# Kernel optimization log

Measured on AMD Instinct MI355X. Metric: run time of the kernel, lower is better.

Reference implementation:

```python
import jax, jax.numpy as jnp
import numpy as np

NUM_HEADS = 16
DIM = 1024


def setup_inputs() -> dict:
    key = jax.random.key(0)
    k1, k2, k3, k4 = jax.random.split(key, 4)
    B, N, C = 4, 2048, DIM
    x = jax.random.normal(k1, (B, N, C), dtype=jnp.float32)
    # weights stored in apply orientation: y = x @ W (+ b)
    W_qkv = jax.random.normal(k2, (C, 3 * C), dtype=jnp.float32) * (C ** -0.5)
    W_out = jax.random.normal(k3, (C, C), dtype=jnp.float32) * (C ** -0.5)
    b_out = jax.random.normal(k4, (C,), dtype=jnp.float32) * 0.01
    return {"hidden_states": x, "W_qkv": W_qkv, "W_out": W_out, "b_out": b_out}


def reference(hidden_states, W_qkv, W_out, b_out):
    B, N, C = hidden_states.shape
    H = NUM_HEADS
    Dh = C // H
    scale = Dh ** -0.5
    qkv = hidden_states @ W_qkv                      # [B, N, 3C]
    qkv = qkv.reshape(B, N, 3, H, Dh).transpose(2, 0, 3, 1, 4)  # [3, B, H, N, Dh]
    q, k, v = qkv[0], qkv[1], qkv[2]
    scores = jnp.einsum('bhnd,bhmd->bhnm', q, k) * scale  # [B, H, N, N]
    probs = jax.nn.softmax(scores, axis=-1)
    out = jnp.einsum('bhnm,bhmd->bhnd', probs, v)    # [B, H, N, Dh]
    out = out.transpose(0, 2, 1, 3).reshape(B, N, C)  # merge heads
    return out @ W_out + b_out                        # dropout p=0 -> identity
```

## Files before the change

kernel.cpp:

```cpp
#include <hip/hip_runtime.h>
#include <hip/hip_bf16.h>
#include <stdint.h>

#define BATCH 4
#define SEQN  2048
#define DIMC  1024
#define NHEADS 16
#define DHEAD 64
#define BH_TOT 64
#define MROWS 8192

typedef __attribute__((ext_vector_type(8))) short bf16x8;
typedef __attribute__((ext_vector_type(4))) float f32x4;

__device__ __forceinline__ unsigned short bf16_rtne(float f){
  union { float f; unsigned u; } v; v.f = f;
  unsigned u = v.u;
  return (unsigned short)((u + 0x7FFFu + ((u >> 16) & 1u)) >> 16);
}
__device__ __forceinline__ float bf16f(unsigned short h){
  union { unsigned u; float f; } v; v.u = ((unsigned)h) << 16;
  return v.f;
}
__device__ __forceinline__ unsigned cvt_pk_bf16(float lo, float hi){
  unsigned r;
  asm("v_cvt_pk_bf16_f32 %0, %1, %2" : "=v"(r) : "v"(lo), "v"(hi));
  return r;
}

__device__ __forceinline__ void async16(void* lds, const void* g){
  __builtin_amdgcn_global_load_lds((const __attribute__((address_space(1))) void*)g,
                                   (__attribute__((address_space(3))) void*)lds, 16, 0, 0);
}

__global__ __launch_bounds__(256) void split_rows_k(const float* __restrict__ X,
    unsigned short* __restrict__ O, int nrows, int Kc){
  int q4 = Kc >> 2;
  int total = nrows * q4;
  int idx = blockIdx.x*256 + threadIdx.x;
  if (idx >= total) return;
  int row = idx / q4, c = idx - row*q4;
  const float4 v = *(const float4*)(X + ((size_t)row*Kc + c*4));
  float fv[4] = {v.x, v.y, v.z, v.w};
  unsigned short hi[4], lo[4];
#pragma unroll
  for (int j=0;j<4;j++){ hi[j] = bf16_rtne(fv[j]); lo[j] = bf16_rtne(fv[j] - bf16f(hi[j])); }
  size_t ob = (size_t)row*(2*Kc) + c*4;
  ushort4 h; h.x=hi[0]; h.y=hi[1]; h.z=hi[2]; h.w=hi[3];
  ushort4 l2; l2.x=lo[0]; l2.y=lo[1]; l2.z=lo[2]; l2.w=lo[3];
  *(ushort4*)(O + ob) = h;
  *(ushort4*)(O + ob + Kc) = l2;
}

__global__ __launch_bounds__(256) void transpose_split_k(const float* __restrict__ W,
    unsigned short* __restrict__ Wt, int K, int Nc){
  __shared__ float tile[32][33];
  int tx = threadIdx.x & 31, ty = threadIdx.x >> 5;
  int n0 = blockIdx.x*32, k0 = blockIdx.y*32;
#pragma unroll
  for (int i=0;i<4;i++){
    int k = k0 + ty + i*8;
    tile[ty + i*8][tx] = W[(size_t)k*Nc + n0 + tx];
  }
  __syncthreads();
#pragma unroll
  for (int i=0;i<4;i++){
    int n = n0 + ty + i*8;
    float f = tile[tx][ty + i*8];
    unsigned short hi = bf16_rtne(f);
    unsigned short lo = bf16_rtne(f - bf16f(hi));
    Wt[(size_t)n*(2*K) + k0 + tx] = hi;
    Wt[(size_t)n*(2*K) + K + k0 + tx] = lo;
  }
}

__global__ __launch_bounds__(512, 4) void gemm_split_k(
    const unsigned short* __restrict__ A, const unsigned short* __restrict__ Bt,
    float* __restrict__ C, const float* __restrict__ bias, int M, int Nc, int K)
{
  __shared__ unsigned short a_lds[3*8192];
  __shared__ unsigned short b_lds[3*4096];
  const int t = threadIdx.x, wid = t>>6, l = t&63, lg = l>>4, ll = l&15;
  const int wm = wid>>1, wn = wid&1;
  const int nbm = M>>8;
  const int nwg = nbm*(Nc>>7);
  const int orig = blockIdx.x;
  const int id = ((orig&7)*(nwg>>3)) + (orig>>3);
  const int m0 = (id % nbm)<<8, n0 = (id / nbm)<<7;
  const int ldk = 2*K;
  const int nkt = (3*K)>>5;
  f32x4 acc[4][4];
#pragma unroll
  for (int i=0;i<4;i++)
#pragma unroll
    for (int j=0;j<4;j++) acc[i][j] = (f32x4){0.f,0.f,0.f,0.f};

  auto stageA = [&](int wb, int kt2){
    const int kp = kt2<<5;
    const int ac = (kp < K) ? kp : kp - K;
#pragma unroll
    for (int i=0;i<2;i++){
      int b = i*8 + wid;
      async16(&a_lds[wb*8192 + b*512 + l*8],
              A + (size_t)(m0 + b*16 + ll)*ldk + ac + lg*8);
    }
  };
  auto stageB = [&](int wb, int kt2){
    const int kp = kt2<<5;
    const int bc = (kp < 2*K) ? kp : kp - 2*K;
    async16(&b_lds[wb*4096 + wid*512 + l*8],
            Bt + (size_t)(n0 + wid*16 + ll)*ldk + bc + lg*8);
  };

  stageA(0, 0); stageB(0, 0);
  stageA(1, 1); stageB(1, 1);

  for (int kt=0; kt<nkt; ++kt){
    if (kt < nkt-1) asm volatile("s_waitcnt vmcnt(3)\n\ts_barrier" ::: "memory");
    else            asm volatile("s_waitcnt vmcnt(0)\n\ts_barrier" ::: "memory");
    const int rb = kt % 3;
    const unsigned short* ab = &a_lds[rb*8192];
    const unsigned short* bb = &b_lds[rb*4096];
    bf16x8 af[4], bf[4];
#pragma unroll
    for (int i=0;i<4;i++) af[i] = *(const bf16x8*)&ab[(wm*4+i)*512 + l*8];
#pragma unroll
    for (int j=0;j<4;j++) bf[j] = *(const bf16x8*)&bb[(wn*4+j)*512 + l*8];
    if (kt+2 < nkt){
      const int wb = (kt+2) % 3;
      stageA(wb, kt+2); stageB(wb, kt+2);
    }
    __builtin_amdgcn_s_setprio(1);
#pragma unroll
    for (int i=0;i<4;i++)
#pragma unroll
      for (int j=0;j<4;j++)
        acc[i][j] = __builtin_amdgcn_mfma_f32_16x16x32_bf16(af[i], bf[j], acc[i][j], 0,0,0);
    __builtin_amdgcn_s_setprio(0);
  }

#pragma unroll
  for (int i=0;i<4;i++)
#pragma unroll
    for (int j=0;j<4;j++){
      int col = n0 + wn*64 + j*16 + ll;
      float bv = bias ? bias[col] : 0.f;
#pragma unroll
      for (int r=0;r<4;r++){
        int row = m0 + wm*64 + i*16 + lg*4 + r;
        C[(size_t)row*Nc + col] = acc[i][j][r] + bv;
      }
    }
}

#define QSCALE 0.18033688f
__global__ __launch_bounds__(256) void split_qk_k(const float* __restrict__ qkv,
    unsigned short* __restrict__ Qo, unsigned short* __restrict__ Ko){
  int idx = blockIdx.x*256 + threadIdx.x;
  int d4 = idx & 15, n = (idx>>4) & (SEQN-1), bh = idx >> 15;
  int b = bh>>4, h = bh&15;
  size_t base = ((size_t)(b*SEQN + n))*3072 + h*64 + d4*4;
  float4 q = *(const float4*)(qkv + base);
  float4 k = *(const float4*)(qkv + base + 1024);
  float fq[4] = {q.x*QSCALE, q.y*QSCALE, q.z*QSCALE, q.w*QSCALE};
  float fk[4] = {k.x, k.y, k.z, k.w};
  unsigned short qh[4], ql[4], kh[4];
#pragma unroll
  for (int j=0;j<4;j++){
    qh[j] = bf16_rtne(fq[j]); ql[j] = bf16_rtne(fq[j] - bf16f(qh[j]));
    kh[j] = bf16_rtne(fk[j]);
  }
  size_t obq = ((size_t)bh*SEQN + n)*128 + d4*4;
  size_t obk = ((size_t)bh*SEQN + n)*64 + d4*4;
  ushort4 u;
  u.x=qh[0];u.y=qh[1];u.z=qh[2];u.w=qh[3]; *(ushort4*)(Qo+obq) = u;
  u.x=ql[0];u.y=ql[1];u.z=ql[2];u.w=ql[3]; *(ushort4*)(Qo+obq+64) = u;
  u.x=kh[0];u.y=kh[1];u.z=kh[2];u.w=kh[3]; *(ushort4*)(Ko+obk) = u;
}

__global__ __launch_bounds__(256) void build_vt_k(const float* __restrict__ qkv,
    unsigned short* __restrict__ Vt){
  __shared__ float tile[64][65];
  const int mt = blockIdx.x, bh = blockIdx.y;
  const int b = bh>>4, h = bh&15;
  const int t = threadIdx.x;
  const int r = t>>2, seg = t&3;
  size_t src = ((size_t)(b*SEQN + mt*64 + r))*3072 + 2048 + h*64 + seg*16;
#pragma unroll
  for (int j=0;j<4;j++){
    float4 v = *(const float4*)(qkv + src + j*4);
    tile[r][seg*16 + j*4 + 0] = v.x;
    tile[r][seg*16 + j*4 + 1] = v.y;
    tile[r][seg*16 + j*4 + 2] = v.z;
    tile[r][seg*16 + j*4 + 3] = v.w;
  }
  __syncthreads();
  const int d = r, ms = seg;
  unsigned short o16[16];
#pragma unroll
  for (int j=0;j<16;j++) o16[j] = bf16_rtne(tile[ms*16 + j][d]);
  size_t dst = ((size_t)(bh*64 + d))*SEQN + mt*64 + ms*16;
  uint4 u0, u1;
  unsigned* pu = (unsigned*)&u0;
  unsigned* pv = (unsigned*)&u1;
#pragma unroll
  for (int j=0;j<4;j++){
    pu[j] = (unsigned)o16[2*j]   | ((unsigned)o16[2*j+1]<<16);
    pv[j] = (unsigned)o16[8+2*j] | ((unsigned)o16[9+2*j]<<16);
  }
  *(uint4*)(Vt + dst) = u0;
  *(uint4*)(Vt + dst + 8) = u1;
}

__global__ __launch_bounds__(256, 4) void attn_k(const unsigned short* __restrict__ Q,
    const unsigned short* __restrict__ Kh, const unsigned short* __restrict__ Vt,
    unsigned short* __restrict__ att_hl)
{
  __shared__ unsigned short k_lds[2][4096];
  __shared__ unsigned short v_lds[2][4096];
  __shared__ unsigned p_lds[4][512];
  const int orig = blockIdx.y*gridDim.x + blockIdx.x;
  const int id = ((orig & 7) << 8) + (orig >> 3);
  const int qt = id & 31, bh = id >> 5;
  const int b = bh>>4, h = bh&15;
  const int t = threadIdx.x, w = t>>6, l = t&63, lg = l>>4, ll = l&15;
  const size_t kvbase = (size_t)bh*SEQN;

  bf16x8 qf[4];
  {
    size_t qrow = (kvbase + qt*64 + w*16 + ll) * 128;
#pragma unroll
    for (int i=0;i<4;i++)
      qf[i] = *(const bf16x8*)(Q + qrow + i*32 + lg*8);
  }
  f32x4 o[4];
#pragma unroll
  for (int d=0; d<4; d++) o[d] = (f32x4){0.f,0.f,0.f,0.f};
  float lsum = 0.f;

  auto stage = [&](int buf, int kv){
    int m0 = kv*64;
#pragma unroll
    for (int i=0;i<2;i++){
      int s = t + i*256; int row = s>>3; int sl = s&7; int sl2 = sl ^ (row&7);
      async16(&k_lds[buf][s*8], Kh + (kvbase + m0 + row)*64 + sl2*8);
    }
#pragma unroll
    for (int i=0;i<2;i++){
      int s = t + i*256; int row = s>>3; int sl = s&7; int sl2 = sl ^ (row&7);
      async16(&v_lds[buf][s*8], Vt + ((size_t)bh*64 + row)*SEQN + m0 + sl2*8);
    }
  };

  stage(0, 0);
  __syncthreads();
  const int NKV = SEQN/64;
  for (int kv=0; kv<NKV; ++kv){
    int cur = kv&1;
    if (kv+1 < NKV) stage(cur^1, kv+1);
#pragma unroll
    for (int nt=0; nt<4; ++nt){
      int row = nt*16 + ll;
      bf16x8 kf0 = *(const bf16x8*)&k_lds[cur][row*64 + (((0*4+lg) ^ (row&7))*8)];
      bf16x8 kf1 = *(const bf16x8*)&k_lds[cur][row*64 + (((1*4+lg) ^ (row&7))*8)];
      f32x4 a = (f32x4){0.f,0.f,0.f,0.f};
      __builtin_amdgcn_s_setprio(1);
      a = __builtin_amdgcn_mfma_f32_16x16x32_bf16(kf0, qf[0], a, 0,0,0);
      a = __builtin_amdgcn_mfma_f32_16x16x32_bf16(kf1, qf[1], a, 0,0,0);
      a = __builtin_amdgcn_mfma_f32_16x16x32_bf16(kf0, qf[2], a, 0,0,0);
      a = __builtin_amdgcn_mfma_f32_16x16x32_bf16(kf1, qf[3], a, 0,0,0);
      __builtin_amdgcn_s_setprio(0);
      float e0 = exp2f(a[0]), e1 = exp2f(a[1]), e2 = exp2f(a[2]), e3 = exp2f(a[3]);
      lsum += (e0 + e1) + (e2 + e3);
      unsigned pk0 = cvt_pk_bf16(e0, e1);
      unsigned pk1 = cvt_pk_bf16(e2, e3);
      int c0 = nt*8 + lg*2;
      int addr = ll*32 + (((c0>>2) ^ (ll&7))<<2) + (c0&3);
      *(uint2*)&p_lds[w][addr] = make_uint2(pk0, pk1);
    }
#pragma unroll
    for (int ks=0; ks<2; ++ks){
      int chunk = ks*4 + lg;
      bf16x8 pf = *(const bf16x8*)&p_lds[w][ll*32 + ((chunk ^ (ll&7))<<2)];
      __builtin_amdgcn_s_setprio(1);
#pragma unroll
      for (int dt=0; dt<4; ++dt){
        int row = dt*16 + ll;
        bf16x8 vf = *(const bf16x8*)&v_lds[cur][row*64 + (((ks*4+lg) ^ (row&7))*8)];
        o[dt] = __builtin_amdgcn_mfma_f32_16x16x32_bf16(pf, vf, o[dt], 0,0,0);
      }
      __builtin_amdgcn_s_setprio(0);
    }
    __syncthreads();
  }
  float tot = lsum;
  tot += __shfl_xor(tot, 16);
  tot += __shfl_xor(tot, 32);
  float inv = 1.0f / tot;
#pragma unroll
  for (int r=0;r<4;r++){
    float rl = __shfl(inv, lg*4 + r);
    int qrow = qt*64 + w*16 + lg*4 + r;
    size_t ob = ((size_t)(b*SEQN + qrow))*2048 + h*64;
#pragma unroll
    for (int dt=0; dt<4; ++dt){
      float f = o[dt][r] * rl;
      unsigned short hi = bf16_rtne(f);
      unsigned short lo = bf16_rtne(f - bf16f(hi));
      att_hl[ob + dt*16 + ll] = hi;
      att_hl[ob + 1024 + dt*16 + ll] = lo;
    }
  }
}

extern "C" void kernel_launch(void* const* d_in, const int* in_sizes, int n_in,
                              void* d_out, int out_size, void* d_ws, size_t ws_size,
                              hipStream_t stream){
  const float* x    = (const float*)d_in[0];
  const float* Wqkv = (const float*)d_in[1];
  const float* Wout = (const float*)d_in[2];
  const float* bout = (const float*)d_in[3];
  float* out = (float*)d_out;

  char* ws = (char*)d_ws;
  size_t off = 0;
  auto walloc = [&](size_t bytes) -> void* {
    void* p = ws + off; off += (bytes + 255) & ~(size_t)255; return p;
  };
  unsigned short* x_hl   = (unsigned short*)walloc((size_t)MROWS*2048*2);
  unsigned short* wqkv_t = (unsigned short*)walloc((size_t)3072*2048*2);
  float*          qkv    = (float*)walloc((size_t)MROWS*3072*4);
  unsigned short* q_hl   = (unsigned short*)walloc((size_t)BH_TOT*SEQN*128*2);
  unsigned short* k_h    = (unsigned short*)walloc((size_t)BH_TOT*SEQN*64*2);
  unsigned short* vt     = (unsigned short*)walloc((size_t)BH_TOT*64*SEQN*2);
  unsigned short* wout_t = (unsigned short*)walloc((size_t)1024*2048*2);
  unsigned short* att_hl = x_hl;

  split_rows_k<<<8192, 256, 0, stream>>>(x, x_hl, MROWS, DIMC);
  transpose_split_k<<<dim3(3072/32, 1024/32), 256, 0, stream>>>(Wqkv, wqkv_t, 1024, 3072);
  transpose_split_k<<<dim3(1024/32, 1024/32), 256, 0, stream>>>(Wout, wout_t, 1024, 1024);
  gemm_split_k<<<768, 512, 0, stream>>>(x_hl, wqkv_t, qkv, nullptr, MROWS, 3072, 1024);
  split_qk_k<<<(BH_TOT*SEQN*16)/256, 256, 0, stream>>>(qkv, q_hl, k_h);
  build_vt_k<<<dim3(SEQN/64, BH_TOT), 256, 0, stream>>>(qkv, vt);
  attn_k<<<dim3(SEQN/64, BH_TOT), 256, 0, stream>>>(q_hl, k_h, vt, att_hl);
  gemm_split_k<<<256, 512, 0, stream>>>(att_hl, wout_t, out, bout, MROWS, 1024, 1024);
}
```

Measured before the change: 559.5 us.

## Retile split-bf16 GEMM to 128x256 tiles with K=64 double-buffered staging

Changes the split-precision GEMM from 256x128 tiles with a 3-stage K=32 ring to 128x256 tiles with K=64 steps and double buffering. A and B loads are interleaved across two half-steps separated by an extra barrier. The warp layout becomes 2x4, and occupancy is lowered to 2 workgroups per CU to fit the larger LDS footprint. The goal is fewer loop iterations and barriers per unit of MFMA work, at the cost of a shallower pipeline and lower occupancy.

New measurement: 556.8 us. Within noise of the previous version (-0.5%).

```diff
diff --git a/kernel.cpp b/kernel.cpp
--- a/kernel.cpp
+++ b/kernel.cpp
@@ -74,81 +74,116 @@
   }
 }
 
-__global__ __launch_bounds__(512, 4) void gemm_split_k(
+__global__ __launch_bounds__(512, 2) void gemm_split_k(
     const unsigned short* __restrict__ A, const unsigned short* __restrict__ Bt,
     float* __restrict__ C, const float* __restrict__ bias, int M, int Nc, int K)
 {
-  __shared__ unsigned short a_lds[3*8192];
-  __shared__ unsigned short b_lds[3*4096];
+  __shared__ unsigned short a_lds[2][8192];
+  __shared__ unsigned short b_lds[2][16384];
   const int t = threadIdx.x, wid = t>>6, l = t&63, lg = l>>4, ll = l&15;
-  const int wm = wid>>1, wn = wid&1;
-  const int nbm = M>>8;
-  const int nwg = nbm*(Nc>>7);
+  const int wm = wid>>2, wn = wid&3;
+  const int nbm = M>>7;
+  const int nwg = nbm*(Nc>>8);
   const int orig = blockIdx.x;
   const int id = ((orig&7)*(nwg>>3)) + (orig>>3);
-  const int m0 = (id % nbm)<<8, n0 = (id / nbm)<<7;
+  const int m0 = (id % nbm)<<7, n0 = (id / nbm)<<8;
   const int ldk = 2*K;
-  const int nkt = (3*K)>>5;
+  const int nkt = (3*K)>>6;
+
   f32x4 acc[4][4];
 #pragma unroll
   for (int i=0;i<4;i++)
 #pragma unroll
     for (int j=0;j<4;j++) acc[i][j] = (f32x4){0.f,0.f,0.f,0.f};
 
-  auto stageA = [&](int wb, int kt2){
-    const int kp = kt2<<5;
+  auto stageA = [&](int kt){
+    const int kp = kt<<6;
     const int ac = (kp < K) ? kp : kp - K;
+    const int buf = kt&1;
 #pragma unroll
     for (int i=0;i<2;i++){
-      int b = i*8 + wid;
-      async16(&a_lds[wb*8192 + b*512 + l*8],
-              A + (size_t)(m0 + b*16 + ll)*ldk + ac + lg*8);
+      int s = i*512 + t;
+      int f = s>>7, kk = (s>>6)&1;
+      async16(&a_lds[buf][s*8],
+              A + (size_t)(m0 + f*16 + ll)*ldk + ac + kk*32 + lg*8);
     }
   };
-  auto stageB = [&](int wb, int kt2){
-    const int kp = kt2<<5;
+  auto stageB = [&](int kt){
+    const int kp = kt<<6;
     const int bc = (kp < 2*K) ? kp : kp - 2*K;
-    async16(&b_lds[wb*4096 + wid*512 + l*8],
-            Bt + (size_t)(n0 + wid*16 + ll)*ldk + bc + lg*8);
+    const int buf = kt&1;
+#pragma unroll
+    for (int g=0; g<2; g++)
+#pragma unroll
+      for (int i=0;i<2;i++){
+        int s = i*512 + t;
+        int fl = s>>7, kk = (s>>6)&1;
+        async16(&b_lds[buf][g*8192 + s*8],
+                Bt + (size_t)(n0 + g*128 + fl*16 + ll)*ldk + bc + kk*32 + lg*8);
+      }
   };
 
-  stageA(0, 0); stageB(0, 0);
-  stageA(1, 1); stageB(1, 1);
+  stageB(0); stageA(0); stageB(1);
+
+  const int bg = wn>>1, bfl0 = (wn&1)*4;
 
   for (int kt=0; kt<nkt; ++kt){
-    if (kt < nkt-1) asm volatile("s_waitcnt vmcnt(3)\n\ts_barrier" ::: "memory");
-    else            asm volatile("s_waitcnt vmcnt(0)\n\ts_barrier" ::: "memory");
-    const int rb = kt % 3;
-    const unsigned short* ab = &a_lds[rb*8192];
-    const unsigned short* bb = &b_lds[rb*4096];
-    bf16x8 af[4], bf[4];
-#pragma unroll
-    for (int i=0;i<4;i++) af[i] = *(const bf16x8*)&ab[(wm*4+i)*512 + l*8];
-#pragma unroll
-    for (int j=0;j<4;j++) bf[j] = *(const bf16x8*)&bb[(wn*4+j)*512 + l*8];
-    if (kt+2 < nkt){
-      const int wb = (kt+2) % 3;
-      stageA(wb, kt+2); stageB(wb, kt+2);
-    }
+    const int buf = kt&1;
+    if (kt < nkt-1) asm volatile("s_waitcnt vmcnt(4)\ns_barrier" ::: "memory");
+    else            asm volatile("s_waitcnt vmcnt(0)\ns_barrier" ::: "memory");
+
+    bf16x8 bfr[4][2];
+#pragma unroll
+    for (int j=0;j<4;j++)
+#pragma unroll
+      for (int kk=0;kk<2;kk++)
+        bfr[j][kk] = *(const bf16x8*)&b_lds[buf][bg*8192 + ((bfl0+j)*2+kk)*512 + l*8];
+    bf16x8 af0[2][2];
+#pragma unroll
+    for (int i=0;i<2;i++)
+#pragma unroll
+      for (int kk=0;kk<2;kk++)
+        af0[i][kk] = *(const bf16x8*)&a_lds[buf][((wm*4+i)*2+kk)*512 + l*8];
+    if (kt+1 < nkt) stageA(kt+1);
     __builtin_amdgcn_s_setprio(1);
 #pragma unroll
-    for (int i=0;i<4;i++)
-#pragma unroll
-      for (int j=0;j<4;j++)
-        acc[i][j] = __builtin_amdgcn_mfma_f32_16x16x32_bf16(af[i], bf[j], acc[i][j], 0,0,0);
+    for (int i=0;i<2;i++)
+#pragma unroll
+      for (int kk=0;kk<2;kk++)
+#pragma unroll
+        for (int j=0;j<4;j++)
+          acc[i][j] = __builtin_amdgcn_mfma_f32_16x16x32_bf16(af0[i][kk], bfr[j][kk], acc[i][j], 0,0,0);
     __builtin_amdgcn_s_setprio(0);
-  }
-
-#pragma unroll
-  for (int i=0;i<4;i++)
+    asm volatile("s_barrier" ::: "memory");
+
+    bf16x8 af1[2][2];
+#pragma unroll
+    for (int i=0;i<2;i++)
+#pragma unroll
+      for (int kk=0;kk<2;kk++)
+        af1[i][kk] = *(const bf16x8*)&a_lds[buf][((wm*4+2+i)*2+kk)*512 + l*8];
+    if (kt+2 < nkt) stageB(kt+2);
+    __builtin_amdgcn_s_setprio(1);
+#pragma unroll
+    for (int i=0;i<2;i++)
+#pragma unroll
+      for (int kk=0;kk<2;kk++)
+#pragma unroll
+        for (int j=0;j<4;j++)
+          acc[2+i][j] = __builtin_amdgcn_mfma_f32_16x16x32_bf16(af1[i][kk], bfr[j][kk], acc[2+i][j], 0,0,0);
+    __builtin_amdgcn_s_setprio(0);
+  }
+
+#pragma unroll
+  for (int mf=0;mf<4;mf++)
 #pragma unroll
     for (int j=0;j<4;j++){
-      int col = n0 + wn*64 + j*16 + ll;
+      int col = n0 + (wn*4+j)*16 + ll;
       float bv = bias ? bias[col] : 0.f;
 #pragma unroll
       for (int r=0;r<4;r++){
-        int row = m0 + wm*64 + i*16 + lg*4 + r;
-        C[(size_t)row*Nc + col] = acc[i][j][r] + bv;
+        int row = m0 + (wm*4+mf)*16 + lg*4 + r;
+        C[(size_t)row*Nc + col] = acc[mf][j][r] + bv;
       }
     }
 }
```
